# Optimization experiments

Measured on AMD Instinct MI355X. Metric: run time of the kernel, lower is better.

The kernel has to match this reference:

```python
import jax, jax.numpy as jnp
import numpy as np
import math

B, S, HID, H = 8, 512, 1024, 16
D = HID // H
ATT_SPAN = 512  # max_position_embeddings


def setup_inputs() -> dict:
    key = jax.random.key(0)
    ks = jax.random.split(key, 12)
    sd = 0.02
    hidden_states = jax.random.normal(ks[0], (B, S, HID), jnp.float32)
    attention_mask = jnp.zeros((B, 1, 1, S), jnp.float32)
    # DeBERTa build_relative_position: rel[i, j] = i - j, shape [1, 1, S, S]
    rel = (jnp.arange(S)[:, None] - jnp.arange(S)[None, :]).astype(jnp.int32)
    relative_pos = rel[None, None]
    Wq = jax.random.normal(ks[1], (HID, HID), jnp.float32) * sd
    bq = jnp.zeros((HID,), jnp.float32)
    Wk = jax.random.normal(ks[2], (HID, HID), jnp.float32) * sd
    bk = jnp.zeros((HID,), jnp.float32)
    Wv = jax.random.normal(ks[3], (HID, HID), jnp.float32) * sd
    bv = jnp.zeros((HID,), jnp.float32)
    Wpk = jax.random.normal(ks[4], (HID, HID), jnp.float32) * sd
    bpk = jnp.zeros((HID,), jnp.float32)
    rel_emb = jax.random.normal(ks[5], (2 * ATT_SPAN, HID), jnp.float32) * sd
    return dict(hidden_states=hidden_states, attention_mask=attention_mask,
                relative_pos=relative_pos, Wq=Wq, bq=bq, Wk=Wk, bk=bk,
                Wv=Wv, bv=bv, Wpk=Wpk, bpk=bpk, rel_emb=rel_emb)


def _fwd(hidden_states, attention_mask, relative_pos, Wq, bq, Wk, bk, Wv, bv, Wpk, bpk, rel_emb):
    b, s, _ = hidden_states.shape

    def proj(x, W, bias):  # [b,s,hid] -> [b,h,s,d]
        return (x @ W.T + bias).reshape(b, s, H, D).transpose(0, 2, 1, 3)

    q = proj(hidden_states, Wq, bq)
    k = proj(hidden_states, Wk, bk)
    v = proj(hidden_states, Wv, bv)

    # content-to-content scores, scaled by sqrt(3*num_heads) as in source
    s_content = jnp.einsum('bhid,bhjd->bhij', q, k) / math.sqrt(3.0 * H)

    # positional projections (source uses pos_key layer for BOTH key and query)
    # rel_emb: [2*ATT_SPAN, HID] -> [H, 2*ATT_SPAN, D]
    pos = (rel_emb @ Wpk.T + bpk).reshape(2 * ATT_SPAN, H, D).transpose(1, 0, 2)

    # c2p: q @ pos^T / sqrt(all_head_size * 3), then gather along last axis
    c2p_full = jnp.einsum('bhid,hpd->bhip', q, pos) / math.sqrt(HID * 3.0)  # [b,h,s,2P]
    c2p_pos = jnp.clip(relative_pos + ATT_SPAN, 0, 2 * ATT_SPAN - 1)
    c2p_pos = jnp.broadcast_to(c2p_pos, (b, H, s, s)).astype(jnp.int32)
    c2p = jnp.take_along_axis(c2p_full, c2p_pos, axis=-1)  # [b,h,s,s]

    # p2c: pos / sqrt(3*H) @ k^T, gather along dim -2 with same index
    p2c_full = jnp.einsum('hpd,bhjd->bhpj', pos / math.sqrt(3.0 * H), k)  # [b,h,2P,s]
    p2c = jnp.take_along_axis(p2c_full, c2p_pos, axis=-2)  # [b,h,s,s]

    score = s_content + c2p + p2c + attention_mask
    probs = jax.nn.softmax(score, axis=-1)  # dropout is identity in eval
    out = jnp.einsum('bhij,bhjd->bhid', probs, v)
    return out.transpose(0, 2, 1, 3).reshape(b, s, HID)


def reference(hidden_states, attention_mask, relative_pos, Wq, bq, Wk, bk, Wv, bv, Wpk, bpk, rel_emb):
    return _fwd(hidden_states, attention_mask, relative_pos, Wq, bq, Wk, bk, Wv, bv, Wpk, bpk, rel_emb)
```

## Files before the change

kernel.cpp:

```cpp
#include <hip/hip_runtime.h>
#include <cstdint>
#include <cstddef>

static constexpr int NB  = 8;
static constexpr int S   = 512;
static constexpr int HID = 1024;
static constexpr int NH  = 16;
static constexpr int DH  = 64;
static constexpr int P2  = 1024;

static constexpr float INV_S1 = 0.14433756729740643f;

typedef __bf16 v8bf  __attribute__((ext_vector_type(8)));
typedef __bf16 v4bf  __attribute__((ext_vector_type(4)));
typedef float  f32x4 __attribute__((ext_vector_type(4)));

#define MFMA16(acc, a, b) acc = __builtin_amdgcn_mfma_f32_16x16x32_bf16(a, b, acc, 0, 0, 0)

#define GLOAD_LDS16(gp, lp) __builtin_amdgcn_global_load_lds( \
    (const __attribute__((address_space(1))) void*)(gp), \
    (__attribute__((address_space(3))) void*)(lp), 16, 0, 0)

__global__ void castall(const float* __restrict__ x,  const float* __restrict__ wq,
                        const float* __restrict__ wk, const float* __restrict__ wv,
                        const float* __restrict__ wpk, const float* __restrict__ rel,
                        __bf16* __restrict__ ob) {
  size_t e = ((size_t)blockIdx.x * 256 + threadIdx.x) * 4;
  if (e >= 9437184) return;
  const float* src; size_t off;
  if (e < 4194304) { src = x; off = e; }
  else {
    int r = (int)((e - 4194304) >> 20);
    off = (e - 4194304) & 1048575;
    src = (r == 0) ? wq : (r == 1) ? wk : (r == 2) ? wv : (r == 3) ? wpk : rel;
  }
  float4 v = *(const float4*)(src + off);
  v4bf o;
  o[0] = (__bf16)v.x; o[1] = (__bf16)v.y; o[2] = (__bf16)v.z; o[3] = (__bf16)v.w;
  *(v4bf*)(ob + e) = o;
}

__launch_bounds__(256, 2)
__global__ void proj_gemm(const __bf16* __restrict__ Xb, const __bf16* __restrict__ Rb,
                          const __bf16* __restrict__ Wqb, const __bf16* __restrict__ Wkb,
                          const __bf16* __restrict__ Wvb, const __bf16* __restrict__ Wpkb,
                          const float* __restrict__ bq, const float* __restrict__ bk_,
                          const float* __restrict__ bv_, const float* __restrict__ bpk,
                          __bf16* __restrict__ qo, __bf16* __restrict__ ko,
                          __bf16* __restrict__ vto, __bf16* __restrict__ po) {
  const int z = blockIdx.z;
  const __bf16* A; const __bf16* W; const float* bias; __bf16* out; int M; float osc;
  if      (z == 0) { A = Xb; W = Wqb;  bias = bq;  out = qo;  M = 4096; osc = INV_S1; }
  else if (z == 1) { A = Xb; W = Wkb;  bias = bk_; out = ko;  M = 4096; osc = 1.0f; }
  else if (z == 2) { A = Xb; W = Wvb;  bias = bv_; out = vto; M = 4096; osc = 1.0f; }
  else             { A = Rb; W = Wpkb; bias = bpk; out = po;  M = 1024; osc = INV_S1; }
  const int m0 = blockIdx.x * 128;
  if (m0 >= M) return;
  const int n0 = blockIdx.y * 128;
  const int K = 1024;

  __shared__ __bf16 Lb[16384];
  __bf16* Al = Lb;
  __bf16* Bl = Lb + 8192;
  const __bf16* FA = (z == 2) ? Bl : Al;
  const __bf16* FB = (z == 2) ? Al : Bl;

  const int t = threadIdx.x;
  const int w = t >> 6, lane = t & 63, q4 = lane >> 4, cc = lane & 15;
  const int wm = w >> 1, wn = w & 1;
  const int srow_in = lane >> 3;
  const int sseg    = ((lane & 7) ^ srow_in) * 8;

  f32x4 acc[4][4] = {};

  for (int k0 = 0; k0 < K; k0 += 64) {
    __syncthreads();
    #pragma unroll
    for (int i = 0; i < 4; i++) {
      int rr = w * 32 + i * 8;
      int gr = rr + srow_in;
      GLOAD_LDS16(&A[(size_t)(m0 + gr) * K + k0 + sseg], &Al[rr * 64]);
      GLOAD_LDS16(&W[(size_t)(n0 + gr) * K + k0 + sseg], &Bl[rr * 64]);
    }
    __syncthreads();
    #pragma unroll
    for (int kk = 0; kk < 2; kk++) {
      v8bf af[4], bfg[4];
      const int phys = ((4 * kk + q4) ^ (cc & 7)) * 8;
      #pragma unroll
      for (int mt = 0; mt < 4; mt++)
        af[mt] = *(const v8bf*)(&FA[(wm * 64 + mt * 16 + cc) * 64 + phys]);
      #pragma unroll
      for (int nt = 0; nt < 4; nt++)
        bfg[nt] = *(const v8bf*)(&FB[(wn * 64 + nt * 16 + cc) * 64 + phys]);
      #pragma unroll
      for (int mt = 0; mt < 4; mt++)
        #pragma unroll
        for (int nt = 0; nt < 4; nt++)
          MFMA16(acc[mt][nt], af[mt], bfg[nt]);
    }
  }

  __syncthreads();
  #pragma unroll
  for (int mt = 0; mt < 4; mt++) {
    float4 bias_r;
    if (z == 2)
      bias_r = *(const float4*)(&bias[n0 + wm * 64 + mt * 16 + q4 * 4]);
    #pragma unroll
    for (int nt = 0; nt < 4; nt++) {
      int cl = wn * 64 + nt * 16 + cc;
      float bc = (z == 2) ? 0.f : bias[n0 + cl];
      #pragma unroll
      for (int r = 0; r < 4; r++) {
        int rl = wm * 64 + mt * 16 + q4 * 4 + r;
        float bsv = (z == 2) ? ((const float*)&bias_r)[r] : bc;
        float val = (acc[mt][nt][r] + bsv) * osc;
        int pc = ((cl >> 3) ^ (rl & 7)) * 8 + (cl & 7);
        Lb[rl * 128 + pc] = (__bf16)val;
      }
    }
  }
  __syncthreads();

  const int row = t & 127;
  const int cb0 = (t >> 7) * 8;
  #pragma unroll
  for (int i = 0; i < 8; i++) {
    int ch = cb0 + i;
    int pc = ch ^ (row & 7);
    v8bf vv = *(const v8bf*)(&Lb[row * 128 + pc * 8]);
    size_t o;
    if (z == 2) {
      int n = n0 + row, m = m0 + ch * 8;
      o = (((size_t)(m >> 9) * 16 + (n >> 6)) * 64 + (n & 63)) * 512 + (m & 511);
    } else if (z < 2) {
      int m = m0 + row, n = n0 + ch * 8;
      o = ((size_t)(m >> 9) * 16 + (n >> 6)) * 32768 + (size_t)(m & 511) * 64 + (n & 63);
    } else {
      int m = m0 + row, n = n0 + ch * 8;
      o = (size_t)(n >> 6) * 65536 + (size_t)m * 64 + (n & 63);
    }
    *(v8bf*)(&out[o]) = vv;
  }
}

__launch_bounds__(256, 4)
__global__ void attn(const __bf16* __restrict__ qb, const __bf16* __restrict__ kb,
                     const __bf16* __restrict__ vtb, const __bf16* __restrict__ posb,
                     const float* __restrict__ mask,
                     __bf16* __restrict__ Op, float2* __restrict__ lm) {
  const int bh = blockIdx.y, b = bh >> 4, h = bh & 15;
  const int i0 = blockIdx.x * 64;
  const int jh = blockIdx.z;

  __shared__ __bf16 Sb[64 * 136];

  const int t = threadIdx.x, w = t >> 6, lane = t & 63, q4 = lane >> 4, cc = lane & 15;
  const int arow = w * 16;
  const size_t bho = (size_t)bh * (S * DH);
  const __bf16* qp  = qb  + bho;
  const __bf16* kp  = kb  + bho;
  const __bf16* vtp = vtb + bho;
  const __bf16* pp  = posb + (size_t)h * (P2 * DH);

  v8bf aq0 = *(const v8bf*)(&qp[(size_t)(i0 + arow + cc) * DH + q4 * 8]);
  v8bf aq1 = *(const v8bf*)(&qp[(size_t)(i0 + arow + cc) * DH + 32 + q4 * 8]);

  f32x4 Oc[4] = {};
  float lrow[4] = {0.f, 0.f, 0.f, 0.f};

#define LDP(d0, d1, U) { int p_ = pw0 + 16 * (U) + cc; p_ = min(max(p_, 0), P2 - 1); \
  const __bf16* pr_ = &pp[(size_t)p_ * DH + q4 * 8]; \
  d0 = *(const v8bf*)pr_; d1 = *(const v8bf*)(pr_ + 32); }
#define LDK(d0, d1, NT) { const __bf16* kr_ = &kp[(size_t)(j0 + (NT) * 16 + cc) * DH + q4 * 8]; \
  d0 = *(const v8bf*)kr_; d1 = *(const v8bf*)(kr_ + 32); }
#define GT(U, P0, P1) { f32x4 g_ = {}; MFMA16(g_, aq0, P0); MFMA16(g_, aq1, P1); \
  _Pragma("unroll") for (int r_ = 0; r_ < 4; r_++) { \
    int jj_ = q4 * 4 + r_ - 16 * (U) - cc + 63; \
    if ((unsigned)jj_ < 64u) Sb[(arow + q4 * 4 + r_) * 136 + jj_ * 2] = (__bf16)(g_[r_] * 0.8660254f); } }
#define HT(U, NT, P0, P1, K0, K1) { f32x4 h_ = {}; MFMA16(h_, P0, K0); MFMA16(h_, P1, K1); \
  _Pragma("unroll") for (int r_ = 0; r_ < 4; r_++) { \
    int ar_ = 16 * (U) + q4 * 4 + r_ + 16 * (NT) + cc - 63; \
    if ((unsigned)ar_ < 16u) Sb[(arow + ar_) * 136 + (16 * (NT) + cc) * 2 + 1] = (__bf16)h_[r_]; } }
#define CT(NT, K0, K1) { f32x4 c_ = {}; MFMA16(c_, aq0, K0); MFMA16(c_, aq1, K1); accc[NT] = c_; }

  for (int jt = jh * 4; jt < jh * 4 + 4; jt++) {
    const int j0 = jt * 64;
    const int pw0 = i0 + arow - j0 + 449;

    float mk[4];
    #pragma unroll
    for (int nt = 0; nt < 4; nt++) mk[nt] = mask[(size_t)b * S + j0 + nt * 16 + cc];

    f32x4 accc[4];
    v8bf p40,p41,p30,p31,p20,p21,p10,p11,p00,p01;
    v8bf k00,k01,k10,k11,k20,k21,k30,k31;

    LDP(p40, p41, 4); LDK(k00, k01, 0);
    LDP(p30, p31, 3); LDK(k10, k11, 1);
    GT(4, p40, p41); HT(4, 0, p40, p41, k00, k01); CT(0, k00, k01);
    LDP(p20, p21, 2); LDK(k20, k21, 2);
    GT(3, p30, p31); HT(3, 0, p30, p31, k00, k01); HT(3, 1, p30, p31, k10, k11); CT(1, k10, k11);
    LDP(p10, p11, 1); LDK(k30, k31, 3);
    GT(2, p20, p21); HT(2, 1, p20, p21, k10, k11); HT(2, 2, p20, p21, k20, k21); CT(2, k20, k21);
    LDP(p00, p01, 0);
    GT(1, p10, p11); HT(1, 2, p10, p11, k20, k21); HT(1, 3, p10, p11, k30, k31); CT(3, k30, k31);
    GT(0, p00, p01); HT(0, 3, p00, p01, k30, k31);

    v8bf vf[2][4];
    #pragma unroll
    for (int kk = 0; kk < 2; kk++)
      #pragma unroll
      for (int dt = 0; dt < 4; dt++)
        vf[kk][dt] = *(const v8bf*)(&vtp[(size_t)(dt * 16 + cc) * S + j0 + kk * 32 + q4 * 8]);

    float p[4][4];
    #pragma unroll
    for (int nt = 0; nt < 4; nt++) {
      int jj = nt * 16 + cc;
      #pragma unroll
      for (int r = 0; r < 4; r++) {
        const __bf16* slot = &Sb[(arow + q4 * 4 + r) * 136 + jj * 2];
        float s = accc[nt][r] + (float)slot[0] + (float)slot[1] + mk[nt];
        float e = __expf(s);
        p[nt][r] = e;
        lrow[r] += e;
      }
    }
    #pragma unroll
    for (int nt = 0; nt < 4; nt++)
      #pragma unroll
      for (int r = 0; r < 4; r++)
        Sb[(arow + q4 * 4 + r) * 136 + nt * 16 + cc] = (__bf16)p[nt][r];

    #pragma unroll
    for (int kk = 0; kk < 2; kk++) {
      v8bf ap = *(const v8bf*)(&Sb[(arow + cc) * 136 + kk * 32 + q4 * 8]);
      #pragma unroll
      for (int dt = 0; dt < 4; dt++)
        MFMA16(Oc[dt], ap, vf[kk][dt]);
    }
  }

  #pragma unroll
  for (int off = 1; off < 16; off <<= 1)
    #pragma unroll
    for (int r = 0; r < 4; r++) lrow[r] += __shfl_xor(lrow[r], off, 64);

  const size_t plane = (size_t)jh * (128 * S);
  #pragma unroll
  for (int r = 0; r < 4; r++) {
    int i = i0 + arow + q4 * 4 + r;
    float rl = 1.0f / lrow[r];
    if (cc == 0) lm[plane + (size_t)bh * S + i] = make_float2(0.f, lrow[r]);
    #pragma unroll
    for (int dt = 0; dt < 4; dt++)
      Op[(plane + (size_t)bh * S + i) * 64 + dt * 16 + cc] = (__bf16)(Oc[dt][r] * rl);
  }
#undef LDP
#undef LDK
#undef GT
#undef HT
#undef CT
}

__global__ void combine(const __bf16* __restrict__ Op, const float2* __restrict__ lm,
                        float* __restrict__ out) {
  int tg = blockIdx.x * 256 + threadIdx.x;
  int gi = tg >> 4;
  int d4 = (tg & 15) * 4;
  int bh = gi >> 9, i = gi & 511, b = bh >> 4, h = bh & 15;
  float2 a = lm[gi];
  float2 c = lm[65536 + gi];
  float mmax = fmaxf(a.x, c.x);
  float w0 = __expf(a.x - mmax) * a.y;
  float w1 = __expf(c.x - mmax) * c.y;
  float inv = 1.0f / (w0 + w1);
  w0 *= inv; w1 *= inv;
  v4bf o0 = *(const v4bf*)(&Op[(size_t)gi * 64 + d4]);
  v4bf o1 = *(const v4bf*)(&Op[(size_t)(4194304) + (size_t)gi * 64 + d4]);
  float4 res;
  res.x = w0 * (float)o0[0] + w1 * (float)o1[0];
  res.y = w0 * (float)o0[1] + w1 * (float)o1[1];
  res.z = w0 * (float)o0[2] + w1 * (float)o1[2];
  res.w = w0 * (float)o0[3] + w1 * (float)o1[3];
  *(float4*)(&out[((size_t)b * S + i) * HID + h * 64 + d4]) = res;
}

extern "C" void kernel_launch(void* const* d_in, const int* in_sizes, int n_in,
                              void* d_out, int out_size, void* d_ws, size_t ws_size,
                              hipStream_t stream) {
  const float* hs   = (const float*)d_in[0];
  const float* mask = (const float*)d_in[1];
  const float* Wq  = (const float*)d_in[3];
  const float* bq  = (const float*)d_in[4];
  const float* Wk  = (const float*)d_in[5];
  const float* bk  = (const float*)d_in[6];
  const float* Wv  = (const float*)d_in[7];
  const float* bv  = (const float*)d_in[8];
  const float* Wpk = (const float*)d_in[9];
  const float* bpk = (const float*)d_in[10];
  const float* rel = (const float*)d_in[11];
  float* out = (float*)d_out;

  char* ws = (char*)d_ws;
  __bf16* cb   = (__bf16*)ws;
  __bf16* Xb   = cb;
  __bf16* Wqb  = cb + 4194304;
  __bf16* Wkb  = cb + 5242880;
  __bf16* Wvb  = cb + 6291456;
  __bf16* Wpkb = cb + 7340032;
  __bf16* Rb   = cb + 8388608;
  __bf16* qb   = (__bf16*)(ws + 18874368);
  __bf16* kb   = (__bf16*)(ws + 27262976);
  __bf16* vtb  = (__bf16*)(ws + 35651584);
  __bf16* posb = (__bf16*)(ws + 44040192);
  __bf16* Op   = (__bf16*)ws;
  float2* lm   = (float2*)(ws + 16777216);

  castall<<<9216, 256, 0, stream>>>(hs, Wq, Wk, Wv, Wpk, rel, cb);

  proj_gemm<<<dim3(32, 8, 4), 256, 0, stream>>>(Xb, Rb, Wqb, Wkb, Wvb, Wpkb,
                                                bq, bk, bv, bpk, qb, kb, vtb, posb);

  attn<<<dim3(8, 128, 2), 256, 0, stream>>>(qb, kb, vtb, posb, mask, Op, lm);

  combine<<<4096, 256, 0, stream>>>(Op, lm, out);
}
```

Measured before the change: 254.4 us.

## Double-buffer score tiles in attention to interleave two key tiles

The attention kernel now processes key tiles in pairs with two shared-memory score buffers and two sets of content-score accumulators. It computes the positional/content scores for both tiles before running softmax and PV for each, giving the scheduler more independent MFMA and load work to overlap. Launch bounds change from 4 to 3 blocks per SM for attn and from 2 to 3 for proj_gemm. The cost is doubled LDS for the score buffer and higher register pressure, which can lower occupancy or cause spills.

```diff
diff --git a/kernel.cpp b/kernel.cpp
--- a/kernel.cpp
+++ b/kernel.cpp
@@ -40,7 +40,7 @@
   *(v4bf*)(ob + e) = o;
 }
 
-__launch_bounds__(256, 2)
+__launch_bounds__(256, 3)
 __global__ void proj_gemm(const __bf16* __restrict__ Xb, const __bf16* __restrict__ Rb,
                           const __bf16* __restrict__ Wqb, const __bf16* __restrict__ Wkb,
                           const __bf16* __restrict__ Wvb, const __bf16* __restrict__ Wpkb,
@@ -145,7 +145,7 @@
   }
 }
 
-__launch_bounds__(256, 4)
+__launch_bounds__(256, 3)
 __global__ void attn(const __bf16* __restrict__ qb, const __bf16* __restrict__ kb,
                      const __bf16* __restrict__ vtb, const __bf16* __restrict__ posb,
                      const float* __restrict__ mask,
@@ -154,7 +154,8 @@
   const int i0 = blockIdx.x * 64;
   const int jh = blockIdx.z;
 
-  __shared__ __bf16 Sb[64 * 136];
+  __shared__ __bf16 SbA[64 * 136];
+  __shared__ __bf16 SbB[64 * 136];
 
   const int t = threadIdx.x, w = t >> 6, lane = t & 63, q4 = lane >> 4, cc = lane & 15;
   const int arow = w * 16;
@@ -173,74 +174,73 @@
 #define LDP(d0, d1, U) { int p_ = pw0 + 16 * (U) + cc; p_ = min(max(p_, 0), P2 - 1); \
   const __bf16* pr_ = &pp[(size_t)p_ * DH + q4 * 8]; \
   d0 = *(const v8bf*)pr_; d1 = *(const v8bf*)(pr_ + 32); }
-#define LDK(d0, d1, NT) { const __bf16* kr_ = &kp[(size_t)(j0 + (NT) * 16 + cc) * DH + q4 * 8]; \
+#define LDK(d0, d1, NT) { const __bf16* kr_ = &kp[(size_t)(j0_ + (NT) * 16 + cc) * DH + q4 * 8]; \
   d0 = *(const v8bf*)kr_; d1 = *(const v8bf*)(kr_ + 32); }
-#define GT(U, P0, P1) { f32x4 g_ = {}; MFMA16(g_, aq0, P0); MFMA16(g_, aq1, P1); \
+#define GT(U, P0, P1, SB) { f32x4 g_ = {}; MFMA16(g_, aq0, P0); MFMA16(g_, aq1, P1); \
   _Pragma("unroll") for (int r_ = 0; r_ < 4; r_++) { \
     int jj_ = q4 * 4 + r_ - 16 * (U) - cc + 63; \
-    if ((unsigned)jj_ < 64u) Sb[(arow + q4 * 4 + r_) * 136 + jj_ * 2] = (__bf16)(g_[r_] * 0.8660254f); } }
-#define HT(U, NT, P0, P1, K0, K1) { f32x4 h_ = {}; MFMA16(h_, P0, K0); MFMA16(h_, P1, K1); \
+    if ((unsigned)jj_ < 64u) SB[(arow + q4 * 4 + r_) * 136 + jj_ * 2] = (__bf16)(g_[r_] * 0.8660254f); } }
+#define HT(U, NT, P0, P1, K0, K1, SB) { f32x4 h_ = {}; MFMA16(h_, P0, K0); MFMA16(h_, P1, K1); \
   _Pragma("unroll") for (int r_ = 0; r_ < 4; r_++) { \
     int ar_ = 16 * (U) + q4 * 4 + r_ + 16 * (NT) + cc - 63; \
-    if ((unsigned)ar_ < 16u) Sb[(arow + ar_) * 136 + (16 * (NT) + cc) * 2 + 1] = (__bf16)h_[r_]; } }
-#define CT(NT, K0, K1) { f32x4 c_ = {}; MFMA16(c_, aq0, K0); MFMA16(c_, aq1, K1); accc[NT] = c_; }
-
-  for (int jt = jh * 4; jt < jh * 4 + 4; jt++) {
-    const int j0 = jt * 64;
-    const int pw0 = i0 + arow - j0 + 449;
-
-    float mk[4];
-    #pragma unroll
-    for (int nt = 0; nt < 4; nt++) mk[nt] = mask[(size_t)b * S + j0 + nt * 16 + cc];
-
-    f32x4 accc[4];
-    v8bf p40,p41,p30,p31,p20,p21,p10,p11,p00,p01;
-    v8bf k00,k01,k10,k11,k20,k21,k30,k31;
-
-    LDP(p40, p41, 4); LDK(k00, k01, 0);
-    LDP(p30, p31, 3); LDK(k10, k11, 1);
-    GT(4, p40, p41); HT(4, 0, p40, p41, k00, k01); CT(0, k00, k01);
-    LDP(p20, p21, 2); LDK(k20, k21, 2);
-    GT(3, p30, p31); HT(3, 0, p30, p31, k00, k01); HT(3, 1, p30, p31, k10, k11); CT(1, k10, k11);
-    LDP(p10, p11, 1); LDK(k30, k31, 3);
-    GT(2, p20, p21); HT(2, 1, p20, p21, k10, k11); HT(2, 2, p20, p21, k20, k21); CT(2, k20, k21);
-    LDP(p00, p01, 0);
-    GT(1, p10, p11); HT(1, 2, p10, p11, k20, k21); HT(1, 3, p10, p11, k30, k31); CT(3, k30, k31);
-    GT(0, p00, p01); HT(0, 3, p00, p01, k30, k31);
-
-    v8bf vf[2][4];
-    #pragma unroll
-    for (int kk = 0; kk < 2; kk++)
-      #pragma unroll
-      for (int dt = 0; dt < 4; dt++)
-        vf[kk][dt] = *(const v8bf*)(&vtp[(size_t)(dt * 16 + cc) * S + j0 + kk * 32 + q4 * 8]);
-
-    float p[4][4];
-    #pragma unroll
-    for (int nt = 0; nt < 4; nt++) {
-      int jj = nt * 16 + cc;
-      #pragma unroll
-      for (int r = 0; r < 4; r++) {
-        const __bf16* slot = &Sb[(arow + q4 * 4 + r) * 136 + jj * 2];
-        float s = accc[nt][r] + (float)slot[0] + (float)slot[1] + mk[nt];
-        float e = __expf(s);
-        p[nt][r] = e;
-        lrow[r] += e;
-      }
-    }
-    #pragma unroll
-    for (int nt = 0; nt < 4; nt++)
-      #pragma unroll
-      for (int r = 0; r < 4; r++)
-        Sb[(arow + q4 * 4 + r) * 136 + nt * 16 + cc] = (__bf16)p[nt][r];
-
-    #pragma unroll
-    for (int kk = 0; kk < 2; kk++) {
-      v8bf ap = *(const v8bf*)(&Sb[(arow + cc) * 136 + kk * 32 + q4 * 8]);
-      #pragma unroll
-      for (int dt = 0; dt < 4; dt++)
-        MFMA16(Oc[dt], ap, vf[kk][dt]);
-    }
+    if ((unsigned)ar_ < 16u) SB[(arow + ar_) * 136 + (16 * (NT) + cc) * 2 + 1] = (__bf16)h_[r_]; } }
+#define CT(NT, K0, K1, ACC) { f32x4 c_ = {}; MFMA16(c_, aq0, K0); MFMA16(c_, aq1, K1); ACC[NT] = c_; }
+
+#define COMPUTE_TILE(J0, SB, ACC) { \
+  const int j0_ = (J0); \
+  const int pw0 = i0 + arow - j0_ + 449; \
+  v8bf p40,p41,p30,p31,p20,p21,p10,p11,p00,p01; \
+  v8bf k00,k01,k10,k11,k20,k21,k30,k31; \
+  LDP(p40, p41, 4); LDK(k00, k01, 0); \
+  LDP(p30, p31, 3); LDK(k10, k11, 1); \
+  GT(4, p40, p41, SB); HT(4, 0, p40, p41, k00, k01, SB); CT(0, k00, k01, ACC); \
+  LDP(p20, p21, 2); LDK(k20, k21, 2); \
+  GT(3, p30, p31, SB); HT(3, 0, p30, p31, k00, k01, SB); HT(3, 1, p30, p31, k10, k11, SB); CT(1, k10, k11, ACC); \
+  LDP(p10, p11, 1); LDK(k30, k31, 3); \
+  GT(2, p20, p21, SB); HT(2, 1, p20, p21, k10, k11, SB); HT(2, 2, p20, p21, k20, k21, SB); CT(2, k20, k21, ACC); \
+  LDP(p00, p01, 0); \
+  GT(1, p10, p11, SB); HT(1, 2, p10, p11, k20, k21, SB); HT(1, 3, p10, p11, k30, k31, SB); CT(3, k30, k31, ACC); \
+  GT(0, p00, p01, SB); HT(0, 3, p00, p01, k30, k31, SB); \
+}
+
+#define SOFT_PV(J0, SB, ACC) { \
+  const int j0_ = (J0); \
+  v8bf vf[2][4]; \
+  _Pragma("unroll") for (int kk = 0; kk < 2; kk++) \
+    _Pragma("unroll") for (int dt = 0; dt < 4; dt++) \
+      vf[kk][dt] = *(const v8bf*)(&vtp[(size_t)(dt * 16 + cc) * S + j0_ + kk * 32 + q4 * 8]); \
+  float mk[4]; \
+  _Pragma("unroll") for (int nt = 0; nt < 4; nt++) mk[nt] = mask[(size_t)b * S + j0_ + nt * 16 + cc]; \
+  float pv[4][4]; \
+  _Pragma("unroll") for (int nt = 0; nt < 4; nt++) { \
+    int jj = nt * 16 + cc; \
+    _Pragma("unroll") for (int r = 0; r < 4; r++) { \
+      const __bf16* slot = &SB[(arow + q4 * 4 + r) * 136 + jj * 2]; \
+      float s = ACC[nt][r] + (float)slot[0] + (float)slot[1] + mk[nt]; \
+      float e = __expf(s); \
+      pv[nt][r] = e; \
+      lrow[r] += e; \
+    } \
+  } \
+  _Pragma("unroll") for (int nt = 0; nt < 4; nt++) \
+    _Pragma("unroll") for (int r = 0; r < 4; r++) \
+      SB[(arow + q4 * 4 + r) * 136 + nt * 16 + cc] = (__bf16)pv[nt][r]; \
+  _Pragma("unroll") for (int kk = 0; kk < 2; kk++) { \
+    v8bf ap = *(const v8bf*)(&SB[(arow + cc) * 136 + kk * 32 + q4 * 8]); \
+    _Pragma("unroll") for (int dt = 0; dt < 4; dt++) \
+      MFMA16(Oc[dt], ap, vf[kk][dt]); \
+  } \
+}
+
+  f32x4 accA[4], accB[4];
+  #pragma unroll
+  for (int u = 0; u < 2; u++) {
+    const int jA = (jh * 4 + 2 * u) * 64;
+    const int jB = jA + 64;
+    COMPUTE_TILE(jA, SbA, accA);
+    COMPUTE_TILE(jB, SbB, accB);
+    SOFT_PV(jA, SbA, accA);
+    SOFT_PV(jB, SbB, accB);
   }
 
   #pragma unroll
@@ -263,6 +263,8 @@
 #undef GT
 #undef HT
 #undef CT
+#undef COMPUTE_TILE
+#undef SOFT_PV
 }
 
 __global__ void combine(const __bf16* __restrict__ Op, const float2* __restrict__ lm,
```

New measurement: 272.8 us. 1.07x slower.
